# Performance work log

Measured on AMD Instinct MI355X. Metric: run time of the kernel, lower is better.

Reference implementation:

```python
import jax, jax.numpy as jnp
import numpy as np

C = 1024
H = 16
EPS = 1e-5

def _layernorm(x, g, b):
    mu = jnp.mean(x, axis=-1, keepdims=True)
    var = jnp.mean(jnp.square(x - mu), axis=-1, keepdims=True)
    return (x - mu) * jax.lax.rsqrt(var + EPS) * g + b

def _mha(xq, xkv, wq, bq, wk, bk, wv, bv, wo, bo, causal):
    B, T, Cm = xq.shape
    Tc = xkv.shape[1]
    d = Cm // H
    q = (xq @ wq + bq).reshape(B, T, H, d)
    k = (xkv @ wk + bk).reshape(B, Tc, H, d)
    v = (xkv @ wv + bv).reshape(B, Tc, H, d)
    att = jnp.einsum('bthd,bshd->bhts', q, k) * (1.0 / np.sqrt(d))
    if causal:
        mask = jnp.tril(jnp.ones((T, Tc), dtype=bool))
        att = jnp.where(mask[None, None], att, -jnp.inf)
    att = jax.nn.softmax(att, axis=-1)
    y = jnp.einsum('bhts,bshd->bthd', att, v).reshape(B, T, Cm)
    return y @ wo + bo


def setup_inputs() -> dict:
    key = jax.random.key(0)
    ks = jax.random.split(key, 20)
    s = 0.02
    w = lambda k: (s * jax.random.normal(k, (C, C))).astype(jnp.float32)
    inp = {
        'x': jax.random.normal(ks[0], (4, 1024, C), dtype=jnp.float32),
        'context': jax.random.normal(ks[1], (4, 1024, C), dtype=jnp.float32),
        'ln1_g': jnp.ones((C,)), 'ln1_b': jnp.zeros((C,)),
        'ln2_g': jnp.ones((C,)), 'ln2_b': jnp.zeros((C,)),
        'sa_wq': w(ks[2]), 'sa_bq': jnp.zeros((C,)),
        'sa_wk': w(ks[3]), 'sa_bk': jnp.zeros((C,)),
        'sa_wv': w(ks[4]), 'sa_bv': jnp.zeros((C,)),
        'sa_wo': w(ks[5]), 'sa_bo': jnp.zeros((C,)),
        'ca_wq': w(ks[6]), 'ca_bq': jnp.zeros((C,)),
        'ca_wk': w(ks[7]), 'ca_bk': jnp.zeros((C,)),
        'ca_wv': w(ks[8]), 'ca_bv': jnp.zeros((C,)),
        'ca_wo': w(ks[9]), 'ca_bo': jnp.zeros((C,)),
        'mlp_w1': (s * jax.random.normal(ks[10], (C, 4 * C))).astype(jnp.float32),
        'mlp_b1': jnp.zeros((4 * C,)),
        'mlp_w2': (s * jax.random.normal(ks[11], (4 * C, C))).astype(jnp.float32),
        'mlp_b2': jnp.zeros((C,)),
    }
    return inp


def reference(x, context, ln1_g, ln1_b, ln2_g, ln2_b,
              sa_wq, sa_bq, sa_wk, sa_bk, sa_wv, sa_bv, sa_wo, sa_bo,
              ca_wq, ca_bq, ca_wk, ca_bk, ca_wv, ca_bv, ca_wo, ca_bo,
              mlp_w1, mlp_b1, mlp_w2, mlp_b2):
    # x = x + self_attn(ln1(x))  (causal)
    x = x + _mha(_layernorm(x, ln1_g, ln1_b), _layernorm(x, ln1_g, ln1_b),
                 sa_wq, sa_bq, sa_wk, sa_bk, sa_wv, sa_bv, sa_wo, sa_bo, causal=True)
    # x = x + cross_attn(ln2(x), context)  (non-causal)
    x = x + _mha(_layernorm(x, ln2_g, ln2_b), context,
                 ca_wq, ca_bq, ca_wk, ca_bk, ca_wv, ca_bv, ca_wo, ca_bo, causal=False)
    # x = x + mlp(ln2(x))  -- note: the module reuses ln2 here (as in source)
    h = _layernorm(x, ln2_g, ln2_b)
    h = jax.nn.gelu(h @ mlp_w1 + mlp_b1, approximate=False) @ mlp_w2 + mlp_b2
    x = x + h
    return x
```

## Files before the change

### kernel.cpp

```cpp
#include <hip/hip_runtime.h>
#include <hip/hip_bf16.h>

typedef __attribute__((ext_vector_type(8))) short s8v;
typedef __attribute__((ext_vector_type(4))) float f4v;

#define DEV static __device__ __forceinline__

DEV unsigned short f2bf(float f) {
    unsigned int u = __builtin_bit_cast(unsigned int, f);
    unsigned int r = u + 0x7FFFu + ((u >> 16) & 1u);
    return (unsigned short)(r >> 16);
}

DEV f4v fzero() { f4v v = {0.f, 0.f, 0.f, 0.f}; return v; }

DEV float fgelu(float x) {
    float z = x * (1.5957691f + 0.07135482f * x * x);
    float s = __builtin_amdgcn_rcpf(1.0f + __expf(-z));
    return x * s;
}

DEV void gload16(const void* g, void* l) {
    __builtin_amdgcn_global_load_lds(
        (const __attribute__((address_space(1))) unsigned int*)g,
        (__attribute__((address_space(3))) unsigned int*)l, 16, 0, 0);
}

struct P8 { const float* p[8]; };
__global__ __launch_bounds__(256) void k_transpose8(
        P8 ws8, unsigned short* __restrict__ base) {
    __shared__ float tile[32][33];
    int z = blockIdx.z;
    const float* W = ws8.p[z];
    unsigned short* Wt = base + (size_t)z * 1024 * 1024;
    int tx = threadIdx.x & 31, ty = threadIdx.x >> 5;
    int n0 = blockIdx.x * 32, k0 = blockIdx.y * 32;
#pragma unroll
    for (int r = 0; r < 32; r += 8)
        tile[ty + r][tx] = W[(size_t)(k0 + ty + r) * 1024 + n0 + tx];
    __syncthreads();
#pragma unroll
    for (int r = 0; r < 32; r += 8)
        Wt[(size_t)(n0 + ty + r) * 1024 + k0 + tx] = f2bf(tile[tx][ty + r]);
}

__global__ __launch_bounds__(256) void k_transpose_bf16(
        const float* __restrict__ W, unsigned short* __restrict__ Wt, int K, int N) {
    __shared__ float tile[32][33];
    int tx = threadIdx.x & 31, ty = threadIdx.x >> 5;
    int n0 = blockIdx.x * 32, k0 = blockIdx.y * 32;
#pragma unroll
    for (int r = 0; r < 32; r += 8)
        tile[ty + r][tx] = W[(size_t)(k0 + ty + r) * N + n0 + tx];
    __syncthreads();
#pragma unroll
    for (int r = 0; r < 32; r += 8)
        Wt[(size_t)(n0 + ty + r) * K + k0 + tx] = f2bf(tile[tx][ty + r]);
}

__global__ __launch_bounds__(256) void k_f32_to_bf16(
        const float* __restrict__ in, unsigned short* __restrict__ out, int n) {
    int i = (blockIdx.x * 256 + threadIdx.x) * 8;
    if (i >= n) return;
    float4 a = *(const float4*)(in + i);
    float4 b = *(const float4*)(in + i + 4);
    uint4 o;
    o.x = f2bf(a.x) | ((unsigned)f2bf(a.y) << 16);
    o.y = f2bf(a.z) | ((unsigned)f2bf(a.w) << 16);
    o.z = f2bf(b.x) | ((unsigned)f2bf(b.y) << 16);
    o.w = f2bf(b.z) | ((unsigned)f2bf(b.w) << 16);
    *(uint4*)(out + i) = o;
}

__global__ __launch_bounds__(256) void k_bias_cat(
        const float* q, const float* k, const float* v,
        const float* k2, const float* v2, float* out) {
    int i = blockIdx.x * 256 + threadIdx.x;
    float val;
    if (i < 1024) val = q[i];
    else if (i < 2048) val = k[i - 1024];
    else if (i < 3072) val = v[i - 2048];
    else if (i < 4096) val = k2[i - 3072];
    else val = v2[i - 4096];
    out[i] = val;
}

__global__ __launch_bounds__(256) void k_layernorm(
        const float* __restrict__ x, const float* __restrict__ g,
        const float* __restrict__ b, unsigned short* __restrict__ out) {
    int row = blockIdx.x;
    int t = threadIdx.x;
    const float* xr = x + (size_t)row * 1024;
    float4 v = *(const float4*)(xr + t * 4);
    float s = v.x + v.y + v.z + v.w;
    float ss = v.x * v.x + v.y * v.y + v.z * v.z + v.w * v.w;
#pragma unroll
    for (int m = 1; m < 64; m <<= 1) { s += __shfl_xor(s, m); ss += __shfl_xor(ss, m); }
    __shared__ float red[16];
    int w = t >> 6;
    if ((t & 63) == 0) { red[w] = s; red[8 + w] = ss; }
    __syncthreads();
    s = red[0] + red[1] + red[2] + red[3];
    ss = red[8] + red[9] + red[10] + red[11];
    float mu = s * (1.f / 1024.f);
    float rstd = rsqrtf(ss * (1.f / 1024.f) - mu * mu + 1e-5f);
    float4 gv = *(const float4*)(g + t * 4);
    float4 bv = *(const float4*)(b + t * 4);
    float y0 = (v.x - mu) * rstd * gv.x + bv.x;
    float y1 = (v.y - mu) * rstd * gv.y + bv.y;
    float y2 = (v.z - mu) * rstd * gv.z + bv.z;
    float y3 = (v.w - mu) * rstd * gv.w + bv.w;
    uint2 o;
    o.x = f2bf(y0) | ((unsigned)f2bf(y1) << 16);
    o.y = f2bf(y2) | ((unsigned)f2bf(y3) << 16);
    *(uint2*)(out + (size_t)row * 1024 + t * 4) = o;
}

template <int EPI, int BM>
__global__ __launch_bounds__(256) void k_gemm(
        const unsigned short* __restrict__ A, const unsigned short* __restrict__ Bt,
        const float* __restrict__ bias, const float* __restrict__ res,
        void* __restrict__ outv, int M, int N, int K) {
    constexpr int WI = (BM == 128) ? 4 : 2;
    constexpr int ABUF = BM * 64;
    constexpr int BUFSZ = ABUF + 8192;
    __shared__ __align__(16) char smem[3 * BUFSZ];
    int nbx = N >> 7;
    int bid = blockIdx.x;
    int cpx = gridDim.x >> 3;
    int swz = (bid & 7) * cpx + (bid >> 3);
    int bx = swz % nbx, by = swz / nbx;
    int m0 = by * BM, n0 = bx << 7;
    int tid = threadIdx.x, w = tid >> 6, l = tid & 63;
    int wr = w >> 1, wc = w & 1;
    int lq = l >> 4, lc = l & 15;
    f4v acc[WI][4];
#pragma unroll
    for (int i = 0; i < WI; ++i)
#pragma unroll
        for (int j = 0; j < 4; ++j) acc[i][j] = fzero();
    const unsigned short* Ab = A + (size_t)m0 * K;
    const unsigned short* Bb = Bt + (size_t)n0 * K;
    int arow = w * 16 + (l >> 2);
    int ach = (((l & 3) ^ ((arow >> 1) & 3)) << 3);

    auto STAGE = [&](int t) {
        int kt = t << 5;
        char* buf = smem + (t % 3) * BUFSZ;
        gload16(Ab + (size_t)arow * K + kt + ach, buf + w * 1024);
        if constexpr (BM == 128)
            gload16(Ab + (size_t)(64 + arow) * K + kt + ach, buf + 4096 + w * 1024);
        gload16(Bb + (size_t)arow * K + kt + ach, buf + ABUF + w * 1024);
        gload16(Bb + (size_t)(64 + arow) * K + kt + ach, buf + ABUF + 4096 + w * 1024);
    };
    int cs = ((lq ^ ((lc >> 1) & 3)) << 4);
    auto COMPUTE = [&](int t) {
        const char* buf = smem + (t % 3) * BUFSZ;
        s8v af[WI], bfr[4];
#pragma unroll
        for (int i = 0; i < WI; ++i)
            af[i] = *(const s8v*)(buf + (wr * (BM / 2) + i * 16 + lc) * 64 + cs);
#pragma unroll
        for (int j = 0; j < 4; ++j)
            bfr[j] = *(const s8v*)(buf + ABUF + (wc * 64 + j * 16 + lc) * 64 + cs);
        __builtin_amdgcn_s_setprio(1);
#pragma unroll
        for (int i = 0; i < WI; ++i)
#pragma unroll
            for (int j = 0; j < 4; ++j)
                acc[i][j] = __builtin_amdgcn_mfma_f32_16x16x32_bf16(af[i], bfr[j], acc[i][j], 0, 0, 0);
        __builtin_amdgcn_s_setprio(0);
    };

    int NT = K >> 5;
    STAGE(0); STAGE(1);
    if constexpr (BM == 128) asm volatile("s_waitcnt vmcnt(4)" ::: "memory");
    else                     asm volatile("s_waitcnt vmcnt(3)" ::: "memory");
    __builtin_amdgcn_s_barrier();
    for (int t = 0; t < NT; ++t) {
        if (t + 2 < NT) STAGE(t + 2);
        COMPUTE(t);
        if (t + 2 < NT) {
            if constexpr (BM == 128) asm volatile("s_waitcnt vmcnt(4)" ::: "memory");
            else                     asm volatile("s_waitcnt vmcnt(3)" ::: "memory");
        } else if (t + 1 < NT) {
            asm volatile("s_waitcnt vmcnt(0)" ::: "memory");
        }
        __builtin_amdgcn_s_barrier();
    }

    float* esc = (float*)smem + w * 1088;
#pragma unroll
    for (int i = 0; i < WI; ++i) {
#pragma unroll
        for (int j = 0; j < 4; ++j)
#pragma unroll
            for (int r = 0; r < 4; ++r)
                esc[(lq * 4 + r) * 68 + j * 16 + lc] = acc[i][j][r];
#pragma unroll
        for (int p = 0; p < 4; ++p) {
            int rr = p * 4 + lq;
            float4 v = *(const float4*)(esc + rr * 68 + lc * 4);
            int row = m0 + wr * (BM / 2) + i * 16 + rr;
            int col = n0 + wc * 64 + lc * 4;
            float4 bv = *(const float4*)(bias + col);
            v.x += bv.x; v.y += bv.y; v.z += bv.z; v.w += bv.w;
            size_t idx = (size_t)row * N + col;
            if (EPI == 0) {
                ushort4 o;
                o.x = f2bf(v.x); o.y = f2bf(v.y); o.z = f2bf(v.z); o.w = f2bf(v.w);
                *(ushort4*)((unsigned short*)outv + idx) = o;
            } else if (EPI == 1) {
                ushort4 o;
                o.x = f2bf(fgelu(v.x)); o.y = f2bf(fgelu(v.y));
                o.z = f2bf(fgelu(v.z)); o.w = f2bf(fgelu(v.w));
                *(ushort4*)((unsigned short*)outv + idx) = o;
            } else {
                float4 rv = *(const float4*)(res + idx);
                v.x += rv.x; v.y += rv.y; v.z += rv.z; v.w += rv.w;
                *(float4*)((float*)outv + idx) = v;
            }
        }
    }
}

template <int EPI>
__global__ __launch_bounds__(256, 2) void k_gemm2(
        const unsigned short* __restrict__ A, const unsigned short* __restrict__ Bt,
        const float* __restrict__ bias, void* __restrict__ outv,
        int M, int N, int K) {
    constexpr int BUFSZ = 8192 + 16384;
    __shared__ __align__(16) char smem[3 * BUFSZ];
    int nbx = N >> 8;
    int bid = blockIdx.x;
    int cpx = gridDim.x >> 3;
    int swz = (bid & 7) * cpx + (bid >> 3);
    int bx = swz % nbx, by = swz / nbx;
    int m0 = by << 7, n0 = bx << 8;
    int tid = threadIdx.x, w = tid >> 6, l = tid & 63;
    int wr = w >> 1, wc = w & 1;
    int lq = l >> 4, lc = l & 15;
    f4v acc[4][8];
#pragma unroll
    for (int i = 0; i < 4; ++i)
#pragma unroll
        for (int j = 0; j < 8; ++j) acc[i][j] = fzero();
    const unsigned short* Ab = A + (size_t)m0 * K;
    const unsigned short* Bb = Bt + (size_t)n0 * K;
    int arow = w * 16 + (l >> 2);
    int ach = (((l & 3) ^ ((arow >> 1) & 3)) << 3);

    auto STAGE_P0 = [&](int t) {
        int kt = t << 5;
        char* buf = smem + (t % 3) * BUFSZ;
        gload16(Ab + (size_t)arow * K + kt + ach, buf + w * 1024);
        gload16(Ab + (size_t)(64 + arow) * K + kt + ach, buf + 4096 + w * 1024);
        gload16(Bb + (size_t)arow * K + kt + ach, buf + 8192 + w * 1024);
        gload16(Bb + (size_t)(64 + arow) * K + kt + ach, buf + 8192 + 4096 + w * 1024);
    };
    auto STAGE_P1 = [&](int t) {
        int kt = t << 5;
        char* buf = smem + (t % 3) * BUFSZ;
        gload16(Bb + (size_t)(128 + arow) * K + kt + ach, buf + 8192 + 8192 + w * 1024);
        gload16(Bb + (size_t)(192 + arow) * K + kt + ach, buf + 8192 + 12288 + w * 1024);
    };
    int cs = ((lq ^ ((lc >> 1) & 3)) << 4);

    int NT = K >> 5;
    STAGE_P0(0); STAGE_P1(0); STAGE_P0(1); STAGE_P1(1);
    asm volatile("s_waitcnt vmcnt(6)" ::: "memory");
    __builtin_amdgcn_s_barrier();
    for (int t = 0; t < NT; ++t) {
        const char* buf = smem + (t % 3) * BUFSZ;
        bool pf = (t + 2 < NT);
        s8v af[4], bfr[8];
#pragma unroll
        for (int i = 0; i < 4; ++i)
            af[i] = *(const s8v*)(buf + (wr * 64 + i * 16 + lc) * 64 + cs);
#pragma unroll
        for (int j = 0; j < 4; ++j)
            bfr[j] = *(const s8v*)(buf + 8192 + (wc * 128 + j * 16 + lc) * 64 + cs);
        if (pf) STAGE_P0(t + 2);
        asm volatile("s_waitcnt lgkmcnt(0)" ::: "memory");
        __builtin_amdgcn_sched_barrier(0);
        __builtin_amdgcn_s_setprio(1);
#pragma unroll
        for (int i = 0; i < 4; ++i)
#pragma unroll
            for (int j = 0; j < 4; ++j)
                acc[i][j] = __builtin_amdgcn_mfma_f32_16x16x32_bf16(af[i], bfr[j], acc[i][j], 0, 0, 0);
        __builtin_amdgcn_s_setprio(0);
#pragma unroll
        for (int j = 4; j < 8; ++j)
            bfr[j] = *(const s8v*)(buf + 8192 + (wc * 128 + j * 16 + lc) * 64 + cs);
        if (pf) STAGE_P1(t + 2);
        asm volatile("s_waitcnt lgkmcnt(0)" ::: "memory");
        __builtin_amdgcn_sched_barrier(0);
        __builtin_amdgcn_s_setprio(1);
#pragma unroll
        for (int i = 0; i < 4; ++i)
#pragma unroll
            for (int j = 4; j < 8; ++j)
                acc[i][j] = __builtin_amdgcn_mfma_f32_16x16x32_bf16(af[i], bfr[j], acc[i][j], 0, 0, 0);
        __builtin_amdgcn_s_setprio(0);
        if (pf) {
            asm volatile("s_waitcnt vmcnt(6)" ::: "memory");
        } else if (t + 1 < NT) {
            asm volatile("s_waitcnt vmcnt(0)" ::: "memory");
        }
        __builtin_amdgcn_s_barrier();
    }

    float* esc = (float*)smem + w * 2112;
#pragma unroll
    for (int i = 0; i < 4; ++i) {
#pragma unroll
        for (int j = 0; j < 8; ++j)
#pragma unroll
            for (int r = 0; r < 4; ++r)
                esc[(lq * 4 + r) * 132 + j * 16 + lc] = acc[i][j][r];
#pragma unroll
        for (int p = 0; p < 4; ++p) {
            int rr = p * 4 + lq;
            int row = m0 + wr * 64 + i * 16 + rr;
#pragma unroll
            for (int h = 0; h < 2; ++h) {
                float4 v = *(const float4*)(esc + rr * 132 + h * 64 + lc * 4);
                int col = n0 + wc * 128 + h * 64 + lc * 4;
                float4 bv = *(const float4*)(bias + col);
                v.x += bv.x; v.y += bv.y; v.z += bv.z; v.w += bv.w;
                size_t idx = (size_t)row * N + col;
                ushort4 o;
                if (EPI == 0) {
                    o.x = f2bf(v.x); o.y = f2bf(v.y); o.z = f2bf(v.z); o.w = f2bf(v.w);
                } else {
                    o.x = f2bf(fgelu(v.x)); o.y = f2bf(fgelu(v.y));
                    o.z = f2bf(fgelu(v.z)); o.w = f2bf(fgelu(v.w));
                }
                *(ushort4*)((unsigned short*)outv + idx) = o;
            }
        }
    }
}

template <bool CAUSAL>
__global__ __launch_bounds__(256) void k_attn(
        const unsigned short* __restrict__ Q, int ldq,
        const unsigned short* __restrict__ Kp, int ldk,
        const unsigned short* __restrict__ Vp, int ldv,
        unsigned short* __restrict__ O, int ldo, int T) {
    __shared__ unsigned short Ks[2][64 * 64];
    __shared__ unsigned short Vt[2][64 * 64];
    __shared__ unsigned short Ps[4][16 * 64];
    int nqt = T >> 6;
    int qt0, qt1, bh;
    if (CAUSAL) {
        int pairs = nqt >> 1;
        int pr = blockIdx.x % pairs;
        bh = blockIdx.x / pairs;
        qt0 = pr; qt1 = nqt - 1 - pr;
    } else {
        qt1 = blockIdx.x % nqt;
        bh = blockIdx.x / nqt;
        qt0 = 0;
    }
    int b = bh >> 4, h = bh & 15;
    int tid = threadIdx.x, w = tid >> 6, l = tid & 63;
    int lq = l >> 4, lc = l & 15;
    size_t qoff = (size_t)b * T * ldq + h * 64;
    size_t koff = (size_t)b * T * ldk + h * 64;
    size_t voff = (size_t)b * T * ldv + h * 64;
    s8v qf1[2], qf0[2];
    {
        const unsigned short* qp = Q + qoff + (size_t)(qt1 * 64 + w * 16 + lc) * ldq + lq * 8;
        qf1[0] = *(const s8v*)qp;
        qf1[1] = *(const s8v*)(qp + 32);
        if (CAUSAL) {
            const unsigned short* q0p = Q + qoff + (size_t)(qt0 * 64 + w * 16 + lc) * ldq + lq * 8;
            qf0[0] = *(const s8v*)q0p;
            qf0[1] = *(const s8v*)(q0p + 32);
        }
    }
    s8v ones;
#pragma unroll
    for (int i = 0; i < 8; ++i) ones[i] = (short)0x3F80;
    f4v o1[4], o0[4];
    float l1r[4], l0r[4];
    float m1 = -3.0e38f, m0 = -3.0e38f;
#pragma unroll
    for (int j = 0; j < 4; ++j) {
        o1[j] = fzero(); o0[j] = fzero(); l1r[j] = 0.f; l0r[j] = 0.f;
    }
    int p = tid & 31, dbase = (tid >> 5) * 8;
    s8v v0r, v1r;

    auto STAGE_K = [&](int kt, int bufi) {
#pragma unroll
        for (int s = 0; s < 2; ++s) {
            int idx = s * 256 + w * 64 + l;
            int t = idx >> 3;
            int ch = (idx & 7) ^ (t & 7);
            gload16(Kp + koff + (size_t)(kt * 64 + t) * ldk + ch * 8,
                    (char*)Ks[bufi] + s * 4096 + w * 1024);
        }
    };
    auto LOAD_V = [&](int kt) {
        const unsigned short* vp = Vp + voff + (size_t)(kt * 64 + 2 * p) * ldv + dbase;
        v0r = *(const s8v*)vp;
        v1r = *(const s8v*)(vp + ldv);
    };
    auto WRITE_V = [&](int bufi) {
#pragma unroll
        for (int j = 0; j < 8; ++j) {
            int dd = dbase + j;
            unsigned int val = (unsigned short)v0r[j] | ((unsigned)(unsigned short)v1r[j] << 16);
            *(unsigned int*)((char*)Vt[bufi] + dd * 128 +
                             ((((p >> 2) ^ (dd & 7)) << 4) | ((p & 3) << 2))) = val;
        }
    };

    const float SC = 0.18033688011112042f;

    auto SMPV = [&](f4v (&sa)[4], f4v (&oa)[4], float& mr, float (&lr)[4],
                    int bufi, int qt, int kt) {
        bool diag = CAUSAL && (kt == qt);
        int qloc = w * 16 + lc;
        float pv[16];
        float tm = -3.0e38f;
#pragma unroll
        for (int jn = 0; jn < 4; ++jn)
#pragma unroll
            for (int j = 0; j < 4; ++j) {
                float sv = sa[jn][j] * SC;
                if (diag && (jn * 16 + lq * 4 + j > qloc)) sv = -3.0e38f;
                pv[jn * 4 + j] = sv;
                tm = fmaxf(tm, sv);
            }
        tm = fmaxf(tm, __shfl_xor(tm, 16));
        tm = fmaxf(tm, __shfl_xor(tm, 32));
        float mnew = fmaxf(mr, tm);
        float alpha = exp2f(mr - mnew);
        mr = mnew;
#pragma unroll
        for (int j = 0; j < 4; ++j) {
            float aj = __shfl(alpha, lq * 4 + j);
            lr[j] *= aj;
#pragma unroll
            for (int jn = 0; jn < 4; ++jn) oa[jn][j] *= aj;
        }
#pragma unroll
        for (int jn = 0; jn < 4; ++jn) {
            int chunk = (jn * 2 + (lq >> 1)) ^ (lc & 7);
            char* basep = (char*)Ps[w] + lc * 128 + (chunk << 4) + ((lq & 1) << 3);
            unsigned e01 = f2bf(exp2f(pv[jn * 4 + 0] - mnew)) |
                           ((unsigned)f2bf(exp2f(pv[jn * 4 + 1] - mnew)) << 16);
            unsigned e23 = f2bf(exp2f(pv[jn * 4 + 2] - mnew)) |
                           ((unsigned)f2bf(exp2f(pv[jn * 4 + 3] - mnew)) << 16);
            *(unsigned*)basep = e01;
            *(unsigned*)(basep + 4) = e23;
        }
        s8v pa[2];
#pragma unroll
        for (int kc = 0; kc < 2; ++kc)
            pa[kc] = *(const s8v*)((const char*)Ps[w] + lc * 128 +
                                   (((kc * 4 + lq) ^ (lc & 7)) << 4));
        f4v sone = fzero();
        __builtin_amdgcn_s_setprio(1);
#pragma unroll
        for (int kc = 0; kc < 2; ++kc) {
            sone = __builtin_amdgcn_mfma_f32_16x16x32_bf16(pa[kc], ones, sone, 0, 0, 0);
#pragma unroll
            for (int jn = 0; jn < 4; ++jn) {
                int dd = jn * 16 + lc;
                s8v bf = *(const s8v*)((const char*)Vt[bufi] + dd * 128 +
                                       (((kc * 4 + lq) ^ (dd & 7)) << 4));
                oa[jn] = __builtin_amdgcn_mfma_f32_16x16x32_bf16(pa[kc], bf, oa[jn], 0, 0, 0);
            }
        }
        __builtin_amdgcn_s_setprio(0);
#pragma unroll
        for (int j = 0; j < 4; ++j) lr[j] += sone[j];
    };

    int ktend = CAUSAL ? (qt1 + 1) : nqt;
    STAGE_K(0, 0); LOAD_V(0);
    asm volatile("s_waitcnt vmcnt(0)" ::: "memory");
    WRITE_V(0);
    __syncthreads();
    int buf = 0;
    for (int kt = 0; kt < ktend; ++kt) {
        bool pf = (kt + 1 < ktend);
        if (pf) { STAGE_K(kt + 1, buf ^ 1); LOAD_V(kt + 1); }
        bool do0 = CAUSAL && (kt <= qt0);
        f4v sa1[4], sa0[4];
        __builtin_amdgcn_s_setprio(1);
#pragma unroll
        for (int jn = 0; jn < 4; ++jn) {
            sa1[jn] = fzero(); sa0[jn] = fzero();
            int t = jn * 16 + lc;
#pragma unroll
            for (int kc = 0; kc < 2; ++kc) {
                s8v kf = *(const s8v*)((const char*)Ks[buf] + t * 128 +
                                       (((kc * 4 + lq) ^ (t & 7)) << 4));
                sa1[jn] = __builtin_amdgcn_mfma_f32_16x16x32_bf16(kf, qf1[kc], sa1[jn], 0, 0, 0);
                if (do0)
                    sa0[jn] = __builtin_amdgcn_mfma_f32_16x16x32_bf16(kf, qf0[kc], sa0[jn], 0, 0, 0);
            }
        }
        __builtin_amdgcn_s_setprio(0);
        SMPV(sa1, o1, m1, l1r, buf, qt1, kt);
        if (do0) SMPV(sa0, o0, m0, l0r, buf, qt0, kt);
        if (pf) {
            asm volatile("s_waitcnt vmcnt(0)" ::: "memory");
            WRITE_V(buf ^ 1);
        }
        __syncthreads();
        buf ^= 1;
    }
#pragma unroll
    for (int j = 0; j < 4; ++j) {
        float inv = 1.0f / l1r[j];
        int row = qt1 * 64 + w * 16 + lq * 4 + j;
#pragma unroll
        for (int jn = 0; jn < 4; ++jn)
            O[(size_t)(b * T + row) * ldo + h * 64 + jn * 16 + lc] = f2bf(o1[jn][j] * inv);
    }
    if (CAUSAL) {
#pragma unroll
        for (int j = 0; j < 4; ++j) {
            float inv = 1.0f / l0r[j];
            int row = qt0 * 64 + w * 16 + lq * 4 + j;
#pragma unroll
            for (int jn = 0; jn < 4; ++jn)
                O[(size_t)(b * T + row) * ldo + h * 64 + jn * 16 + lc] = f2bf(o0[jn][j] * inv);
        }
    }
}

extern "C" void kernel_launch(void* const* d_in, const int* in_sizes, int n_in,
                              void* d_out, int out_size, void* d_ws, size_t ws_size,
                              hipStream_t stream) {
    const float* x     = (const float*)d_in[0];
    const float* ctx   = (const float*)d_in[1];
    const float* ln1_g = (const float*)d_in[2];
    const float* ln1_b = (const float*)d_in[3];
    const float* ln2_g = (const float*)d_in[4];
    const float* ln2_b = (const float*)d_in[5];
    const float* sa_wq = (const float*)d_in[6];  const float* sa_bq = (const float*)d_in[7];
    const float* sa_wk = (const float*)d_in[8];  const float* sa_bk = (const float*)d_in[9];
    const float* sa_wv = (const float*)d_in[10]; const float* sa_bv = (const float*)d_in[11];
    const float* sa_wo = (const float*)d_in[12]; const float* sa_bo = (const float*)d_in[13];
    const float* ca_wq = (const float*)d_in[14]; const float* ca_bq = (const float*)d_in[15];
    const float* ca_wk = (const float*)d_in[16]; const float* ca_bk = (const float*)d_in[17];
    const float* ca_wv = (const float*)d_in[18]; const float* ca_bv = (const float*)d_in[19];
    const float* ca_wo = (const float*)d_in[20]; const float* ca_bo = (const float*)d_in[21];
    const float* w1 = (const float*)d_in[22]; const float* b1 = (const float*)d_in[23];
    const float* w2 = (const float*)d_in[24]; const float* b2 = (const float*)d_in[25];
    float* out = (float*)d_out;

    char* ws = (char*)d_ws;
    const size_t MB = 1024 * 1024;
    unsigned short* wt_base = (unsigned short*)(ws + 0 * MB);
    unsigned short* wt_saq = wt_base + 0 * 1024 * 1024;
    unsigned short* wt_cak = wt_base + 5 * 1024 * 1024;
    unsigned short* wt_sao = wt_base + 3 * 1024 * 1024;
    unsigned short* wt_caq = wt_base + 4 * 1024 * 1024;
    unsigned short* wt_cao = wt_base + 7 * 1024 * 1024;
    unsigned short* w1t    = (unsigned short*)(ws + 16 * MB);
    unsigned short* w2t    = (unsigned short*)(ws + 24 * MB);
    unsigned short* ctxb   = (unsigned short*)(ws + 32 * MB);
    float*          x1     = (float*)        (ws + 40 * MB);
    unsigned short* qbuf   = (unsigned short*)(ws + 56 * MB);
    unsigned short* kbuf   = (unsigned short*)(ws + 64 * MB);
    unsigned short* hln    = (unsigned short*)(ws + 80 * MB);
    float*          bcat   = (float*)        (ws + 88 * MB);
    unsigned short* qkv = qbuf;
    unsigned short* kv  = kbuf;
    unsigned short* m1  = qbuf;
    unsigned short* h3  = ctxb;

    dim3 blk(256);
    P8 ws8;
    ws8.p[0] = sa_wq; ws8.p[1] = sa_wk; ws8.p[2] = sa_wv; ws8.p[3] = sa_wo;
    ws8.p[4] = ca_wq; ws8.p[5] = ca_wk; ws8.p[6] = ca_wv; ws8.p[7] = ca_wo;
    k_transpose8<<<dim3(32, 32, 8), blk, 0, stream>>>(ws8, wt_base);
    k_transpose_bf16<<<dim3(128, 32), blk, 0, stream>>>(w1, w1t, 1024, 4096);
    k_transpose_bf16<<<dim3(32, 128), blk, 0, stream>>>(w2, w2t, 4096, 1024);
    k_f32_to_bf16<<<dim3(2048), blk, 0, stream>>>(ctx, ctxb, 4 * 1024 * 1024);
    k_bias_cat<<<dim3(20), blk, 0, stream>>>(sa_bq, sa_bk, sa_bv, ca_bk, ca_bv, bcat);

    k_layernorm<<<dim3(4096), blk, 0, stream>>>(x, ln1_g, ln1_b, hln);
    k_gemm2<0><<<dim3(32 * 12), blk, 0, stream>>>(hln, wt_saq, bcat, qkv, 4096, 3072, 1024);
    k_attn<true><<<dim3(512), blk, 0, stream>>>(qkv, 3072, qkv + 1024, 3072, qkv + 2048, 3072,
                                                hln, 1024, 1024);
    k_gemm<2, 64><<<dim3(64 * 8), blk, 0, stream>>>(hln, wt_sao, sa_bo, x, x1, 4096, 1024, 1024);

    k_layernorm<<<dim3(4096), blk, 0, stream>>>(x1, ln2_g, ln2_b, hln);
    k_gemm<0, 64><<<dim3(64 * 8), blk, 0, stream>>>(hln, wt_caq, ca_bq, nullptr, qbuf, 4096, 1024, 1024);
    k_gemm<0, 128><<<dim3(16 * 32), blk, 0, stream>>>(ctxb, wt_cak, bcat + 3072, nullptr, kv, 4096, 2048, 1024);
    k_attn<false><<<dim3(1024), blk, 0, stream>>>(qbuf, 1024, kv, 2048, kv + 1024, 2048,
                                                  hln, 1024, 1024);
    k_gemm<2, 64><<<dim3(64 * 8), blk, 0, stream>>>(hln, wt_cao, ca_bo, x1, out, 4096, 1024, 1024);

    k_layernorm<<<dim3(4096), blk, 0, stream>>>(out, ln2_g, ln2_b, h3);
    k_gemm2<1><<<dim3(32 * 16), blk, 0, stream>>>(h3, w1t, b1, m1, 4096, 4096, 1024);
    k_gemm<2, 64><<<dim3(64 * 8), blk, 0, stream>>>(m1, w2t, b2, out, out, 4096, 1024, 4096);
}
```

Before: 346.3 us.

## Fold softmax scale into Q projection, lazy rescale, packed bf16 convert in attention

Moves the softmax scale (1/sqrt(d)*log2e) into the Q-projection GEMM epilogue so attention skips a multiply per score. The online-softmax rescale of the accumulator is now skipped unless the running max grows by more than 8 (log2 units) anywhere in the wave. Probability bf16 packing uses the hardware v_cvt_pk_bf16_f32 instruction instead of manual rounding. Bf16 rounding of Q now happens after scaling, and the lazy max lets exponentials reach up to 2^8, which slightly changes numerics and the overflow margin.

```diff
diff --git a/kernel.cpp b/kernel.cpp
--- a/kernel.cpp
+++ b/kernel.cpp
@@ -5,6 +5,8 @@
 typedef __attribute__((ext_vector_type(4))) float f4v;
 
 #define DEV static __device__ __forceinline__
+
+__device__ const float SCQ = 0.18033688011112042f;
 
 DEV unsigned short f2bf(float f) {
     unsigned int u = __builtin_bit_cast(unsigned int, f);
@@ -120,7 +122,7 @@
 __global__ __launch_bounds__(256) void k_gemm(
         const unsigned short* __restrict__ A, const unsigned short* __restrict__ Bt,
         const float* __restrict__ bias, const float* __restrict__ res,
-        void* __restrict__ outv, int M, int N, int K) {
+        void* __restrict__ outv, int M, int N, int K, int scaleN) {
     constexpr int WI = (BM == 128) ? 4 : 2;
     constexpr int ABUF = BM * 64;
     constexpr int BUFSZ = ABUF + 8192;
@@ -207,8 +209,10 @@
             v.x += bv.x; v.y += bv.y; v.z += bv.z; v.w += bv.w;
             size_t idx = (size_t)row * N + col;
             if (EPI == 0) {
+                float scl = (col < scaleN) ? SCQ : 1.0f;
                 ushort4 o;
-                o.x = f2bf(v.x); o.y = f2bf(v.y); o.z = f2bf(v.z); o.w = f2bf(v.w);
+                o.x = f2bf(v.x * scl); o.y = f2bf(v.y * scl);
+                o.z = f2bf(v.z * scl); o.w = f2bf(v.w * scl);
                 *(ushort4*)((unsigned short*)outv + idx) = o;
             } else if (EPI == 1) {
                 ushort4 o;
@@ -228,7 +232,7 @@
 __global__ __launch_bounds__(256, 2) void k_gemm2(
         const unsigned short* __restrict__ A, const unsigned short* __restrict__ Bt,
         const float* __restrict__ bias, void* __restrict__ outv,
-        int M, int N, int K) {
+        int M, int N, int K, int scaleN) {
     constexpr int BUFSZ = 8192 + 16384;
     __shared__ __align__(16) char smem[3 * BUFSZ];
     int nbx = N >> 8;
@@ -332,7 +336,9 @@
                 size_t idx = (size_t)row * N + col;
                 ushort4 o;
                 if (EPI == 0) {
-                    o.x = f2bf(v.x); o.y = f2bf(v.y); o.z = f2bf(v.z); o.w = f2bf(v.w);
+                    float scl = (col < scaleN) ? SCQ : 1.0f;
+                    o.x = f2bf(v.x * scl); o.y = f2bf(v.y * scl);
+                    o.z = f2bf(v.z * scl); o.w = f2bf(v.w * scl);
                 } else {
                     o.x = f2bf(fgelu(v.x)); o.y = f2bf(fgelu(v.y));
                     o.z = f2bf(fgelu(v.z)); o.w = f2bf(fgelu(v.w));
@@ -419,8 +425,6 @@
         }
     };
 
-    const float SC = 0.18033688011112042f;
-
     auto SMPV = [&](f4v (&sa)[4], f4v (&oa)[4], float& mr, float (&lr)[4],
                     int bufi, int qt, int kt) {
         bool diag = CAUSAL && (kt == qt);
@@ -431,33 +435,38 @@
         for (int jn = 0; jn < 4; ++jn)
 #pragma unroll
             for (int j = 0; j < 4; ++j) {
-                float sv = sa[jn][j] * SC;
+                float sv = sa[jn][j];
                 if (diag && (jn * 16 + lq * 4 + j > qloc)) sv = -3.0e38f;
                 pv[jn * 4 + j] = sv;
                 tm = fmaxf(tm, sv);
             }
         tm = fmaxf(tm, __shfl_xor(tm, 16));
         tm = fmaxf(tm, __shfl_xor(tm, 32));
-        float mnew = fmaxf(mr, tm);
-        float alpha = exp2f(mr - mnew);
-        mr = mnew;
-#pragma unroll
-        for (int j = 0; j < 4; ++j) {
-            float aj = __shfl(alpha, lq * 4 + j);
-            lr[j] *= aj;
-#pragma unroll
-            for (int jn = 0; jn < 4; ++jn) oa[jn][j] *= aj;
+        if (!__all(tm <= mr + 8.0f)) {
+            float mnew = fmaxf(mr, tm);
+            float alpha = exp2f(mr - mnew);
+            mr = mnew;
+#pragma unroll
+            for (int j = 0; j < 4; ++j) {
+                float aj = __shfl(alpha, lq * 4 + j);
+                lr[j] *= aj;
+#pragma unroll
+                for (int jn = 0; jn < 4; ++jn) oa[jn][j] *= aj;
+            }
         }
 #pragma unroll
         for (int jn = 0; jn < 4; ++jn) {
+            float e0 = exp2f(pv[jn * 4 + 0] - mr);
+            float e1 = exp2f(pv[jn * 4 + 1] - mr);
+            float e2 = exp2f(pv[jn * 4 + 2] - mr);
+            float e3 = exp2f(pv[jn * 4 + 3] - mr);
+            unsigned r0, r1;
+            asm("v_cvt_pk_bf16_f32 %0, %1, %2" : "=v"(r0) : "v"(e0), "v"(e1));
+            asm("v_cvt_pk_bf16_f32 %0, %1, %2" : "=v"(r1) : "v"(e2), "v"(e3));
             int chunk = (jn * 2 + (lq >> 1)) ^ (lc & 7);
             char* basep = (char*)Ps[w] + lc * 128 + (chunk << 4) + ((lq & 1) << 3);
-            unsigned e01 = f2bf(exp2f(pv[jn * 4 + 0] - mnew)) |
-                           ((unsigned)f2bf(exp2f(pv[jn * 4 + 1] - mnew)) << 16);
-            unsigned e23 = f2bf(exp2f(pv[jn * 4 + 2] - mnew)) |
-                           ((unsigned)f2bf(exp2f(pv[jn * 4 + 3] - mnew)) << 16);
-            *(unsigned*)basep = e01;
-            *(unsigned*)(basep + 4) = e23;
+            uint2 rr; rr.x = r0; rr.y = r1;
+            *(uint2*)basep = rr;
         }
         s8v pa[2];
 #pragma unroll
@@ -590,19 +599,19 @@
     k_bias_cat<<<dim3(20), blk, 0, stream>>>(sa_bq, sa_bk, sa_bv, ca_bk, ca_bv, bcat);
 
     k_layernorm<<<dim3(4096), blk, 0, stream>>>(x, ln1_g, ln1_b, hln);
-    k_gemm2<0><<<dim3(32 * 12), blk, 0, stream>>>(hln, wt_saq, bcat, qkv, 4096, 3072, 1024);
+    k_gemm2<0><<<dim3(32 * 12), blk, 0, stream>>>(hln, wt_saq, bcat, qkv, 4096, 3072, 1024, 1024);
     k_attn<true><<<dim3(512), blk, 0, stream>>>(qkv, 3072, qkv + 1024, 3072, qkv + 2048, 3072,
                                                 hln, 1024, 1024);
-    k_gemm<2, 64><<<dim3(64 * 8), blk, 0, stream>>>(hln, wt_sao, sa_bo, x, x1, 4096, 1024, 1024);
+    k_gemm<2, 64><<<dim3(64 * 8), blk, 0, stream>>>(hln, wt_sao, sa_bo, x, x1, 4096, 1024, 1024, 0);
 
     k_layernorm<<<dim3(4096), blk, 0, stream>>>(x1, ln2_g, ln2_b, hln);
-    k_gemm<0, 64><<<dim3(64 * 8), blk, 0, stream>>>(hln, wt_caq, ca_bq, nullptr, qbuf, 4096, 1024, 1024);
-    k_gemm<0, 128><<<dim3(16 * 32), blk, 0, stream>>>(ctxb, wt_cak, bcat + 3072, nullptr, kv, 4096, 2048, 1024);
+    k_gemm<0, 64><<<dim3(64 * 8), blk, 0, stream>>>(hln, wt_caq, ca_bq, nullptr, qbuf, 4096, 1024, 1024, 1024);
+    k_gemm<0, 128><<<dim3(16 * 32), blk, 0, stream>>>(ctxb, wt_cak, bcat + 3072, nullptr, kv, 4096, 2048, 1024, 0);
     k_attn<false><<<dim3(1024), blk, 0, stream>>>(qbuf, 1024, kv, 2048, kv + 1024, 2048,
                                                   hln, 1024, 1024);
-    k_gemm<2, 64><<<dim3(64 * 8), blk, 0, stream>>>(hln, wt_cao, ca_bo, x1, out, 4096, 1024, 1024);
+    k_gemm<2, 64><<<dim3(64 * 8), blk, 0, stream>>>(hln, wt_cao, ca_bo, x1, out, 4096, 1024, 1024, 0);
 
     k_layernorm<<<dim3(4096), blk, 0, stream>>>(out, ln2_g, ln2_b, h3);
-    k_gemm2<1><<<dim3(32 * 16), blk, 0, stream>>>(h3, w1t, b1, m1, 4096, 4096, 1024);
-    k_gemm<2, 64><<<dim3(64 * 8), blk, 0, stream>>>(m1, w2t, b2, out, out, 4096, 1024, 4096);
-}
+    k_gemm2<1><<<dim3(32 * 16), blk, 0, stream>>>(h3, w1t, b1, m1, 4096, 4096, 1024, 0);
+    k_gemm<2, 64><<<dim3(64 * 8), blk, 0, stream>>>(m1, w2t, b2, out, out, 4096, 1024, 4096, 0);
+}
```

After: 336.0 us. 3.0% less time.
